# Optimization experiments

Hardware: AMD Instinct MI355X
Metric: run time of the kernel (lower is better)

Reference implementation:

```python
import jax, jax.numpy as jnp
import numpy as np

V, D, H, L, E, DH, K, PMAX = 50257, 128, 4, 4, 8, 512, 2, 256
B, T = 8, 256


def setup_inputs() -> dict:
    key = jax.random.key(0)
    ks = jax.random.split(key, 10)
    s = 0.02
    def n(k, shape):
        return jax.random.normal(k, shape, jnp.float32) * s
    return dict(
        idx=jax.random.randint(ks[0], (B, T), 0, V),
        tok_emb=n(ks[1], (V, D)),
        pos_emb=n(ks[2], (PMAX, D)),
        ln1_g=jnp.ones((L, D), jnp.float32), ln1_b=jnp.zeros((L, D), jnp.float32),
        in_w=n(ks[3], (L, 3 * D, D)), in_b=jnp.zeros((L, 3 * D), jnp.float32),
        out_w=n(ks[4], (L, D, D)), out_b=jnp.zeros((L, D), jnp.float32),
        ln2_g=jnp.ones((L, D), jnp.float32), ln2_b=jnp.zeros((L, D), jnp.float32),
        gate_w=n(ks[5], (L, E, D)),
        w1=n(ks[6], (L, E, DH, D)),
        w2=n(ks[7], (L, E, D, DH)),
        lnf_g=jnp.ones((D,), jnp.float32), lnf_b=jnp.zeros((D,), jnp.float32),
        lm_w=n(ks[8], (V, D)),
    )


def _ln(x, g, b):
    mu = x.mean(-1, keepdims=True)
    var = jnp.var(x, -1, keepdims=True)
    return (x - mu) / jnp.sqrt(var + 1e-5) * g + b


def _moe(x, gw, w1, w2):
    # x: [N, D]; top-2 sparse MoE, computed densely per expert then combined.
    logits = x @ gw.T                              # [N, E]
    probs = jax.nn.softmax(logits, -1)
    topw, topi = jax.lax.top_k(probs, K)           # [N, K]
    topw = topw / topw.sum(-1, keepdims=True)
    we = (topw[..., None] * jax.nn.one_hot(topi, E, dtype=x.dtype)).sum(1)  # [N, E]
    h = jax.nn.silu(jnp.einsum('nd,ehd->neh', x, w1))   # [N, E, DH]
    y = jnp.einsum('neh,edh->ned', h, w2)               # [N, E, D]
    return jnp.einsum('ned,ne->nd', y, we)


def reference(idx, tok_emb, pos_emb, ln1_g, ln1_b, in_w, in_b, out_w, out_b,
              ln2_g, ln2_b, gate_w, w1, w2, lnf_g, lnf_b, lm_w):
    b, t = idx.shape
    x = tok_emb[idx] + pos_emb[:t]                 # [B, T, D]
    dh = D // H
    scale = 1.0 / np.sqrt(dh)
    for l in range(L):
        xl = _ln(x, ln1_g[l], ln1_b[l])
        qkv = xl @ in_w[l].T + in_b[l]
        q, k, v = jnp.split(qkv, 3, -1)
        q = q.reshape(b, t, H, dh)
        k = k.reshape(b, t, H, dh)
        v = v.reshape(b, t, H, dh)
        att = jax.nn.softmax(jnp.einsum('bqhd,bkhd->bhqk', q, k) * scale, -1)
        o = jnp.einsum('bhqk,bkhd->bqhd', att, v).reshape(b, t, D)
        x = x + o @ out_w[l].T + out_b[l]
        x2 = _ln(x, ln2_g[l], ln2_b[l]).reshape(b * t, D)
        x = x + _moe(x2, gate_w[l], w1[l], w2[l]).reshape(b, t, D)
    return _ln(x, lnf_g, lnf_b) @ lm_w.T           # [B, T, V]
```

## Files before the change

### kernel.cpp

```cpp
#include <hip/hip_runtime.h>
#include <math.h>

#define NTOK 2048
#define DD   128
#define NHEAD 4
#define DHEAD 32
#define NLAYER 4
#define NEXP 8
#define DHID 512
#define NVOCAB 50257
#define VPAD  50304
#define SEQ   256
#define NBATCH 8

typedef __attribute__((ext_vector_type(8))) short short8v;
typedef __attribute__((ext_vector_type(4))) float f32x4;

__device__ __forceinline__ unsigned short nm_bf16r(float f) {
  unsigned u = __float_as_uint(f);
  u += 0x7fffu + ((u >> 16) & 1u);
  return (unsigned short)(u >> 16);
}

__device__ __forceinline__ float nm_silu(float a) {
  return a / (1.f + __expf(-a));
}

template<int N4>
__device__ __forceinline__ float nm_dotv(const float* __restrict__ a,
                                         const float* __restrict__ w) {
  const float4* a4 = (const float4*)a;
  const float4* w4 = (const float4*)w;
  float sx = 0.f, sy = 0.f, sz = 0.f, sw = 0.f;
#pragma unroll 16
  for (int k = 0; k < N4; ++k) {
    float4 av = a4[k], wv = w4[k];
    sx = fmaf(av.x, wv.x, sx);
    sy = fmaf(av.y, wv.y, sy);
    sz = fmaf(av.z, wv.z, sz);
    sw = fmaf(av.w, wv.w, sw);
  }
  return (sx + sy) + (sz + sw);
}

__global__ void nm_embed_ln(const int* __restrict__ idx, const float* __restrict__ tok,
                            const float* __restrict__ pos, const float* __restrict__ g,
                            const float* __restrict__ b, float* __restrict__ x,
                            float* __restrict__ xl) {
  int n = blockIdx.x, lane = threadIdx.x;
  int t = idx[n];
  float v0 = tok[(size_t)t * DD + lane]      + pos[(n % SEQ) * DD + lane];
  float v1 = tok[(size_t)t * DD + lane + 64] + pos[(n % SEQ) * DD + lane + 64];
  x[n * DD + lane]      = v0;
  x[n * DD + lane + 64] = v1;
  float s = v0 + v1;
#pragma unroll
  for (int o = 32; o > 0; o >>= 1) s += __shfl_xor(s, o, 64);
  float mu = s * (1.f / 128.f);
  float d0 = v0 - mu, d1 = v1 - mu;
  float q = d0 * d0 + d1 * d1;
#pragma unroll
  for (int o = 32; o > 0; o >>= 1) q += __shfl_xor(q, o, 64);
  float rstd = rsqrtf(q * (1.f / 128.f) + 1e-5f);
  xl[n * DD + lane]      = d0 * rstd * g[lane]      + b[lane];
  xl[n * DD + lane + 64] = d1 * rstd * g[lane + 64] + b[lane + 64];
}

__global__ void nm_ln(const float* __restrict__ in, const float* __restrict__ g,
                      const float* __restrict__ b, float* __restrict__ out) {
  int n = blockIdx.x, lane = threadIdx.x;
  float v0 = in[n * DD + lane], v1 = in[n * DD + lane + 64];
  float s = v0 + v1;
#pragma unroll
  for (int o = 32; o > 0; o >>= 1) s += __shfl_xor(s, o, 64);
  float mu = s * (1.f / 128.f);
  float d0 = v0 - mu, d1 = v1 - mu;
  float q = d0 * d0 + d1 * d1;
#pragma unroll
  for (int o = 32; o > 0; o >>= 1) q += __shfl_xor(q, o, 64);
  float rstd = rsqrtf(q * (1.f / 128.f) + 1e-5f);
  out[n * DD + lane]      = d0 * rstd * g[lane]      + b[lane];
  out[n * DD + lane + 64] = d1 * rstd * g[lane + 64] + b[lane + 64];
}

__global__ void nm_combine_ln(const float* __restrict__ yb, const int* __restrict__ posm,
                              const float* __restrict__ topw, float* __restrict__ x,
                              const float* __restrict__ g, const float* __restrict__ b,
                              float* __restrict__ xl, unsigned short* __restrict__ xb) {
  int n = blockIdx.x, lane = threadIdx.x;
  float w0 = topw[2 * n], w1 = topw[2 * n + 1];
  int p0 = posm[2 * n], p1 = posm[2 * n + 1];
  float v0 = x[n * DD + lane]      + w0 * yb[(size_t)p0 * DD + lane]
                                   + w1 * yb[(size_t)p1 * DD + lane];
  float v1 = x[n * DD + lane + 64] + w0 * yb[(size_t)p0 * DD + lane + 64]
                                   + w1 * yb[(size_t)p1 * DD + lane + 64];
  x[n * DD + lane]      = v0;
  x[n * DD + lane + 64] = v1;
  float s = v0 + v1;
#pragma unroll
  for (int o = 32; o > 0; o >>= 1) s += __shfl_xor(s, o, 64);
  float mu = s * (1.f / 128.f);
  float d0 = v0 - mu, d1 = v1 - mu;
  float q = d0 * d0 + d1 * d1;
#pragma unroll
  for (int o = 32; o > 0; o >>= 1) q += __shfl_xor(q, o, 64);
  float rstd = rsqrtf(q * (1.f / 128.f) + 1e-5f);
  float o0 = d0 * rstd * g[lane]      + b[lane];
  float o1 = d1 * rstd * g[lane + 64] + b[lane + 64];
  xl[n * DD + lane]      = o0;
  xl[n * DD + lane + 64] = o1;
  if (xb) {
    xb[n * DD + lane]      = nm_bf16r(o0);
    xb[n * DD + lane + 64] = nm_bf16r(o1);
  }
}

template<int F>
__global__ __launch_bounds__(256) void nm_gemm(
    const float* __restrict__ A, const float* __restrict__ B,
    float* __restrict__ C, const float* __restrict__ bias,
    int M, int N, int K,
    const int* __restrict__ list, const int* __restrict__ cnt,
    const int* __restrict__ off) {
  constexpr bool GA = F & 1, SI = F & 2, BI = F & 4, RE = F & 8, GR = F & 16;
  __shared__ __align__(16) float As[64][68];
  __shared__ __align__(16) float Bs[64][68];
  int tid = threadIdx.x;
  int n0 = blockIdx.x * 64, m0 = blockIdx.y * 64;
  int Mloc = M, o = 0;
  const float* Bb = B;
  if constexpr (GR) {
    int e = blockIdx.z;
    Mloc = cnt[e];
    if (m0 >= Mloc) return;
    o = off[e];
    Bb = B + (size_t)e * (size_t)N * K;
  }
  int tm = tid & 15, tn = tid >> 4;
  float acc[4][4] = {};
  for (int kc = 0; kc < K; kc += 64) {
#pragma unroll
    for (int i = 0; i < 4; ++i) {
      int f = tid + 256 * i;
      int r = f >> 4, c4 = f & 15;
      int mi = m0 + r;
      if (mi >= Mloc) mi = m0;
      const float* ar;
      if constexpr (GA) ar = A + (size_t)(list[o + mi] >> 1) * K;
      else              ar = A + (size_t)(o + mi) * K;
      float4 v = *(const float4*)(ar + kc + c4 * 4);
      int k = c4 * 4;
      As[k][r] = v.x; As[k + 1][r] = v.y; As[k + 2][r] = v.z; As[k + 3][r] = v.w;
    }
#pragma unroll
    for (int i = 0; i < 4; ++i) {
      int f = tid + 256 * i;
      int r = f >> 4, c4 = f & 15;
      const float* br = Bb + (size_t)(n0 + r) * K + kc + c4 * 4;
      float4 v = *(const float4*)br;
      int k = c4 * 4;
      Bs[k][r] = v.x; Bs[k + 1][r] = v.y; Bs[k + 2][r] = v.z; Bs[k + 3][r] = v.w;
    }
    __syncthreads();
#pragma unroll 16
    for (int k = 0; k < 64; ++k) {
      float4 a = *(const float4*)&As[k][tm * 4];
      float4 b = *(const float4*)&Bs[k][tn * 4];
      acc[0][0] = fmaf(a.x, b.x, acc[0][0]); acc[0][1] = fmaf(a.x, b.y, acc[0][1]);
      acc[0][2] = fmaf(a.x, b.z, acc[0][2]); acc[0][3] = fmaf(a.x, b.w, acc[0][3]);
      acc[1][0] = fmaf(a.y, b.x, acc[1][0]); acc[1][1] = fmaf(a.y, b.y, acc[1][1]);
      acc[1][2] = fmaf(a.y, b.z, acc[1][2]); acc[1][3] = fmaf(a.y, b.w, acc[1][3]);
      acc[2][0] = fmaf(a.z, b.x, acc[2][0]); acc[2][1] = fmaf(a.z, b.y, acc[2][1]);
      acc[2][2] = fmaf(a.z, b.z, acc[2][2]); acc[2][3] = fmaf(a.z, b.w, acc[2][3]);
      acc[3][0] = fmaf(a.w, b.x, acc[3][0]); acc[3][1] = fmaf(a.w, b.y, acc[3][1]);
      acc[3][2] = fmaf(a.w, b.z, acc[3][2]); acc[3][3] = fmaf(a.w, b.w, acc[3][3]);
    }
    __syncthreads();
  }
  float4 bv = {0.f, 0.f, 0.f, 0.f};
  if constexpr (BI) bv = *(const float4*)(bias + n0 + tn * 4);
#pragma unroll
  for (int i = 0; i < 4; ++i) {
    int mi = m0 + tm * 4 + i;
    if (GR && mi >= Mloc) continue;
    float* cr = C + (size_t)(o + mi) * N + n0 + tn * 4;
    float r0 = acc[i][0], r1 = acc[i][1], r2 = acc[i][2], r3 = acc[i][3];
    if constexpr (BI) { r0 += bv.x; r1 += bv.y; r2 += bv.z; r3 += bv.w; }
    if constexpr (SI) { r0 = nm_silu(r0); r1 = nm_silu(r1); r2 = nm_silu(r2); r3 = nm_silu(r3); }
    if constexpr (RE) { r0 += cr[0]; r1 += cr[1]; r2 += cr[2]; r3 += cr[3]; }
    float4 st = {r0, r1, r2, r3};
    *(float4*)cr = st;
  }
}

__global__ __launch_bounds__(256) void nm_oplng(
    const float* __restrict__ ao, const float* __restrict__ w,
    const float* __restrict__ bias, float* __restrict__ x,
    const float* __restrict__ g, const float* __restrict__ b,
    float* __restrict__ xl, const float* __restrict__ gw,
    int* __restrict__ topi, float* __restrict__ topw, int* __restrict__ cnt) {
  __shared__ __align__(16) float As[64][36];
  __shared__ __align__(16) float Bs[64][132];
  __shared__ float Ls[32][9];
  int tid = threadIdx.x;
  int m0 = blockIdx.x * 32;
  int tm = tid >> 5, tn = tid & 31;
  float acc[4][4] = {};
  for (int kc = 0; kc < DD; kc += 64) {
#pragma unroll
    for (int i = 0; i < 2; ++i) {
      int ch = tid + 256 * i, r = ch >> 4, c4 = ch & 15;
      float4 v = *(const float4*)(ao + (size_t)(m0 + r) * DD + kc + c4 * 4);
      int k = c4 * 4;
      As[k][r] = v.x; As[k + 1][r] = v.y; As[k + 2][r] = v.z; As[k + 3][r] = v.w;
    }
#pragma unroll
    for (int i = 0; i < 8; ++i) {
      int ch = tid + 256 * i, r = ch >> 4, c4 = ch & 15;
      float4 v = *(const float4*)(w + (size_t)r * DD + kc + c4 * 4);
      int k = c4 * 4;
      Bs[k][r] = v.x; Bs[k + 1][r] = v.y; Bs[k + 2][r] = v.z; Bs[k + 3][r] = v.w;
    }
    __syncthreads();
#pragma unroll 8
    for (int k = 0; k < 64; ++k) {
      float4 a = *(const float4*)&As[k][tm * 4];
      float4 bb = *(const float4*)&Bs[k][tn * 4];
      acc[0][0] = fmaf(a.x, bb.x, acc[0][0]); acc[0][1] = fmaf(a.x, bb.y, acc[0][1]);
      acc[0][2] = fmaf(a.x, bb.z, acc[0][2]); acc[0][3] = fmaf(a.x, bb.w, acc[0][3]);
      acc[1][0] = fmaf(a.y, bb.x, acc[1][0]); acc[1][1] = fmaf(a.y, bb.y, acc[1][1]);
      acc[1][2] = fmaf(a.y, bb.z, acc[1][2]); acc[1][3] = fmaf(a.y, bb.w, acc[1][3]);
      acc[2][0] = fmaf(a.z, bb.x, acc[2][0]); acc[2][1] = fmaf(a.z, bb.y, acc[2][1]);
      acc[2][2] = fmaf(a.z, bb.z, acc[2][2]); acc[2][3] = fmaf(a.z, bb.w, acc[2][3]);
      acc[3][0] = fmaf(a.w, bb.x, acc[3][0]); acc[3][1] = fmaf(a.w, bb.y, acc[3][1]);
      acc[3][2] = fmaf(a.w, bb.z, acc[3][2]); acc[3][3] = fmaf(a.w, bb.w, acc[3][3]);
    }
    __syncthreads();
  }
  float4 bv = *(const float4*)(bias + tn * 4);
  float rr[4][4], s1[4], s2[4];
#pragma unroll
  for (int i = 0; i < 4; ++i) {
    int rw = m0 + tm * 4 + i;
    float4 xv = *(const float4*)(x + (size_t)rw * DD + tn * 4);
    float r0 = acc[i][0] + bv.x + xv.x;
    float r1 = acc[i][1] + bv.y + xv.y;
    float r2 = acc[i][2] + bv.z + xv.z;
    float r3 = acc[i][3] + bv.w + xv.w;
    rr[i][0] = r0; rr[i][1] = r1; rr[i][2] = r2; rr[i][3] = r3;
    float4 st = {r0, r1, r2, r3};
    *(float4*)(x + (size_t)rw * DD + tn * 4) = st;
    s1[i] = r0 + r1 + r2 + r3;
    s2[i] = r0 * r0 + r1 * r1 + r2 * r2 + r3 * r3;
  }
#pragma unroll
  for (int o = 16; o >= 1; o >>= 1) {
#pragma unroll
    for (int i = 0; i < 4; ++i) {
      s1[i] += __shfl_xor(s1[i], o, 64);
      s2[i] += __shfl_xor(s2[i], o, 64);
    }
  }
  float4 gv  = *(const float4*)(g + tn * 4);
  float4 bbv = *(const float4*)(b + tn * 4);
#pragma unroll
  for (int i = 0; i < 4; ++i) {
    int rw = m0 + tm * 4 + i;
    float mu = s1[i] * (1.f / 128.f);
    float var = s2[i] * (1.f / 128.f) - mu * mu;
    float rstd = rsqrtf(var + 1e-5f);
    float y0 = (rr[i][0] - mu) * rstd * gv.x + bbv.x;
    float y1 = (rr[i][1] - mu) * rstd * gv.y + bbv.y;
    float y2 = (rr[i][2] - mu) * rstd * gv.z + bbv.z;
    float y3 = (rr[i][3] - mu) * rstd * gv.w + bbv.w;
    float4 yv = {y0, y1, y2, y3};
    *(float4*)(xl + (size_t)rw * DD + tn * 4) = yv;
    *(float4*)&Bs[tm * 4 + i][tn * 4] = yv;
  }
  __syncthreads();
  int grow = tid >> 3, ge = tid & 7;
  const float4* xr = (const float4*)&Bs[grow][0];
  const float4* wr = (const float4*)(gw + (size_t)ge * DD);
  float sx = 0.f, sy = 0.f, sz = 0.f, sw = 0.f;
#pragma unroll
  for (int k2 = 0; k2 < 32; ++k2) {
    float4 a = xr[k2], w4 = wr[k2];
    sx = fmaf(a.x, w4.x, sx); sy = fmaf(a.y, w4.y, sy);
    sz = fmaf(a.z, w4.z, sz); sw = fmaf(a.w, w4.w, sw);
  }
  Ls[grow][ge] = (sx + sy) + (sz + sw);
  __syncthreads();
  if (ge == 0) {
    float gl[NEXP];
#pragma unroll
    for (int e = 0; e < NEXP; ++e) gl[e] = Ls[grow][e];
    int i0 = 0;
#pragma unroll
    for (int e = 1; e < NEXP; ++e) if (gl[e] > gl[i0]) i0 = e;
    int i1 = (i0 == 0) ? 1 : 0;
#pragma unroll
    for (int e = 0; e < NEXP; ++e) { if (e != i0 && gl[e] > gl[i1]) i1 = e; }
    float p1 = __expf(gl[i1] - gl[i0]);
    float inv = 1.f / (1.f + p1);
    int n = m0 + grow;
    topi[2 * n] = i0; topi[2 * n + 1] = i1;
    topw[2 * n] = inv; topw[2 * n + 1] = p1 * inv;
    atomicAdd(cnt + i0, 1);
    atomicAdd(cnt + i1, 1);
  }
}

__global__ __launch_bounds__(256) void nm_attn2(const float* __restrict__ qkv,
                                                float* __restrict__ o) {
  __shared__ __align__(16) float Ks[SEQ][DHEAD];
  __shared__ __align__(16) float Vs[SEQ][DHEAD];
  __shared__ float mbuf[32][9], sbuf[32][9];
  __shared__ __align__(16) float accbuf[32][36];
  int bh = blockIdx.x;
  int b = bh >> 2, h = bh & 3;
  int qt = blockIdx.y;
  int tid = threadIdx.x;
  const float* base = qkv + (size_t)b * SEQ * 384;
  for (int f = tid; f < SEQ * 8; f += 256) {
    int t = f >> 3, c4 = f & 7;
    float4 kv = *(const float4*)(base + (size_t)t * 384 + 128 + h * DHEAD + c4 * 4);
    float4 vv = *(const float4*)(base + (size_t)t * 384 + 256 + h * DHEAD + c4 * 4);
    *(float4*)&Ks[t][c4 * 4] = kv;
    *(float4*)&Vs[t][c4 * 4] = vv;
  }
  __syncthreads();
  int q = tid & 31, slot = tid >> 5;
  int tq = qt * 32 + q;
  float qv[DHEAD];
  const float4* q4 = (const float4*)(base + (size_t)tq * 384 + h * DHEAD);
#pragma unroll
  for (int k = 0; k < 8; ++k) {
    float4 v = q4[k];
    qv[4*k] = v.x; qv[4*k+1] = v.y; qv[4*k+2] = v.z; qv[4*k+3] = v.w;
  }
  float m = -1e30f, s = 0.f, acc[DHEAD];
#pragma unroll
  for (int d = 0; d < DHEAD; ++d) acc[d] = 0.f;
  const float scale = 0.17677669529663687f;
  int j0 = slot * 32;
  for (int jj = 0; jj < 32; ++jj) {
    int j = j0 + jj;
    const float4* kr = (const float4*)Ks[j];
    float sc = 0.f;
#pragma unroll
    for (int k = 0; k < 8; ++k) {
      float4 v = kr[k];
      sc += qv[4*k]*v.x + qv[4*k+1]*v.y + qv[4*k+2]*v.z + qv[4*k+3]*v.w;
    }
    sc *= scale;
    float mn = fmaxf(m, sc);
    float f = __expf(m - mn), p = __expf(sc - mn);
    s = s * f + p;
    const float4* vr = (const float4*)Vs[j];
#pragma unroll
    for (int k = 0; k < 8; ++k) {
      float4 v = vr[k];
      acc[4*k]   = acc[4*k]  * f + p * v.x;
      acc[4*k+1] = acc[4*k+1]* f + p * v.y;
      acc[4*k+2] = acc[4*k+2]* f + p * v.z;
      acc[4*k+3] = acc[4*k+3]* f + p * v.w;
    }
    m = mn;
  }
  mbuf[q][slot] = m;
  sbuf[q][slot] = s;
  __syncthreads();
  float M = mbuf[q][0];
#pragma unroll
  for (int t = 1; t < 8; ++t) M = fmaxf(M, mbuf[q][t]);
  float S = 0.f;
#pragma unroll
  for (int t = 0; t < 8; ++t) S += sbuf[q][t] * __expf(mbuf[q][t] - M);
  float w = __expf(m - M);
#pragma unroll
  for (int d = 0; d < DHEAD; ++d) acc[d] *= w;
#pragma unroll
  for (int p = 0; p < 8; ++p) {
    if (slot == p) {
      if (p == 0) {
#pragma unroll
        for (int d = 0; d < DHEAD; ++d) accbuf[q][d] = acc[d];
      } else {
#pragma unroll
        for (int d = 0; d < DHEAD; ++d) accbuf[q][d] += acc[d];
      }
    }
    __syncthreads();
  }
  if (slot == 0) sbuf[q][8] = 1.f / S;
  __syncthreads();
  int q2 = tid >> 3, c4 = tid & 7;
  float inv = sbuf[q2][8];
  float4 v = *(const float4*)&accbuf[q2][c4 * 4];
  v.x *= inv; v.y *= inv; v.z *= inv; v.w *= inv;
  *(float4*)(o + (size_t)(b * SEQ + qt * 32 + q2) * DD + h * DHEAD + c4 * 4) = v;
}

__global__ void nm_route(const int* __restrict__ topi, const int* __restrict__ cnt,
                         int* __restrict__ off, int* __restrict__ list,
                         int* __restrict__ posm) {
  __shared__ int lcur[NEXP];
  int tid = threadIdx.x;
  if (tid < NEXP) {
    int o = 0;
    for (int e = 0; e < tid; ++e) o += cnt[e];
    lcur[tid] = o;
    off[tid] = o;
  }
  __syncthreads();
  for (int t = tid; t < 2 * NTOK; t += 1024) {
    int e = topi[t];
    int p = atomicAdd(&lcur[e], 1);
    list[p] = t;
    posm[t] = p;
  }
}

__global__ void nm_zero(int* __restrict__ p, int n) {
  int i = blockIdx.x * 64 + threadIdx.x;
  if (i < n) p[i] = 0;
}

__global__ void nm_moe(const float* __restrict__ x2, const float* __restrict__ gw,
                       const float* __restrict__ w1, const float* __restrict__ w2,
                       float* __restrict__ x) {
  __shared__ __align__(16) float xs[DD];
  __shared__ __align__(16) float hs[DHID];
  __shared__ float gl[NEXP];
  __shared__ int   ei[2];
  __shared__ float ew[2];
  int n = blockIdx.x, tid = threadIdx.x;
  if (tid < DD) xs[tid] = x2[n * DD + tid];
  __syncthreads();
  if (tid < NEXP) gl[tid] = nm_dotv<32>(xs, gw + (size_t)tid * DD);
  __syncthreads();
  if (tid == 0) {
    int i0 = 0;
#pragma unroll
    for (int e = 1; e < NEXP; ++e) if (gl[e] > gl[i0]) i0 = e;
    int i1 = (i0 == 0) ? 1 : 0;
    for (int e = 0; e < NEXP; ++e) { if (e == i0) continue; if (gl[e] > gl[i1]) i1 = e; }
    float p1 = __expf(gl[i1] - gl[i0]);
    float inv = 1.f / (1.f + p1);
    ei[0] = i0; ei[1] = i1; ew[0] = inv; ew[1] = p1 * inv;
  }
  __syncthreads();
  float yacc = 0.f;
  for (int t2 = 0; t2 < 2; ++t2) {
    int e = ei[t2];
    float wt = ew[t2];
    const float* w1e = w1 + (size_t)e * DHID * DD;
#pragma unroll
    for (int jj = 0; jj < 2; ++jj) {
      int j = tid + jj * 256;
      float a = nm_dotv<32>(xs, w1e + (size_t)j * DD);
      hs[j] = nm_silu(a);
    }
    __syncthreads();
    if (tid < DD) yacc += wt * nm_dotv<128>(hs, w2 + ((size_t)e * DD + tid) * DHID);
    __syncthreads();
  }
  if (tid < DD) x[n * DD + tid] += yacc;
}

__global__ void nm_cvt_w(const float* __restrict__ in, unsigned short* __restrict__ ob) {
  size_t i = (size_t)blockIdx.x * 256 + threadIdx.x;
  const size_t n = (size_t)NVOCAB * DD;
  ob[i] = (i < n) ? nm_bf16r(in[i]) : (unsigned short)0;
}

__device__ __forceinline__ short8v nm_cvt8(const float* p) {
  const float4* p4 = (const float4*)p;
  float4 a = p4[0], b = p4[1];
  short8v r;
  r[0] = (short)nm_bf16r(a.x); r[1] = (short)nm_bf16r(a.y);
  r[2] = (short)nm_bf16r(a.z); r[3] = (short)nm_bf16r(a.w);
  r[4] = (short)nm_bf16r(b.x); r[5] = (short)nm_bf16r(b.y);
  r[6] = (short)nm_bf16r(b.z); r[7] = (short)nm_bf16r(b.w);
  return r;
}

__global__ __launch_bounds__(256) void nm_lmhead2(
    const unsigned short* __restrict__ xfb, const unsigned short* __restrict__ lmwb,
    float* __restrict__ out) {
  __shared__ unsigned short Ab[128 * 128];
  __shared__ unsigned short Bb[128 * 128];
  int tid = threadIdx.x;
  int row0 = blockIdx.y * 128, col0 = blockIdx.x * 128;
#pragma unroll
  for (int i = 0; i < 8; ++i) {
    int ch = tid + i * 256;
    int r = ch >> 4, s = ch & 15;
    int sg = s ^ (r & 7);
    *(short8v*)&Ab[r * 128 + s * 8] =
        *(const short8v*)(xfb + (size_t)(row0 + r) * DD + sg * 8);
    *(short8v*)&Bb[r * 128 + s * 8] =
        *(const short8v*)(lmwb + (size_t)(col0 + r) * DD + sg * 8);
  }
  __syncthreads();
  int wave = tid >> 6, lane = tid & 63;
  int wr = wave >> 1, wc = wave & 1;
  int lr = lane & 15, hk = lane >> 4;
  f32x4 acc[4][4] = {};
#pragma unroll
  for (int ks = 0; ks < 4; ++ks) {
    int sg = ks * 4 + hk;
    int sx = (sg ^ (lr & 7)) * 8;
    short8v a[4], b[4];
#pragma unroll
    for (int i = 0; i < 4; ++i)
      a[i] = *(const short8v*)&Ab[(wr * 64 + i * 16 + lr) * 128 + sx];
#pragma unroll
    for (int j = 0; j < 4; ++j)
      b[j] = *(const short8v*)&Bb[(wc * 64 + j * 16 + lr) * 128 + sx];
#pragma unroll
    for (int i = 0; i < 4; ++i)
#pragma unroll
      for (int j = 0; j < 4; ++j)
        acc[i][j] = __builtin_amdgcn_mfma_f32_16x16x32_bf16(a[i], b[j], acc[i][j], 0, 0, 0);
  }
  int cr = (lane >> 4) * 4;
#pragma unroll
  for (int j = 0; j < 4; ++j) {
    int c = col0 + wc * 64 + j * 16 + (lane & 15);
    if (c < NVOCAB) {
#pragma unroll
      for (int i = 0; i < 4; ++i)
#pragma unroll
        for (int r = 0; r < 4; ++r)
          out[(size_t)(row0 + wr * 64 + i * 16 + cr + r) * NVOCAB + c] = acc[i][j][r];
    }
  }
}

__global__ __launch_bounds__(256) void nm_lmhead_f32(
    const float* __restrict__ xf, const float* __restrict__ lmw,
    float* __restrict__ out) {
  int wave = threadIdx.x >> 6, lane = threadIdx.x & 63;
  int wr = wave >> 1, wc = wave & 1;
  int row0 = blockIdx.y * 128 + wr * 64;
  int col0 = blockIdx.x * 128 + wc * 64;
  int lr = lane & 15, lk = (lane >> 4) * 8;
  f32x4 acc[4][4] = {};
#pragma unroll
  for (int ks = 0; ks < 4; ++ks) {
    int kb = ks * 32 + lk;
    short8v a[4], b[4];
#pragma unroll
    for (int i = 0; i < 4; ++i)
      a[i] = nm_cvt8(xf + (size_t)(row0 + i * 16 + lr) * DD + kb);
#pragma unroll
    for (int j = 0; j < 4; ++j) {
      int c = col0 + j * 16 + lr;
      if (c < NVOCAB) b[j] = nm_cvt8(lmw + (size_t)c * DD + kb);
      else {
        short8v z;
#pragma unroll
        for (int e = 0; e < 8; ++e) z[e] = 0;
        b[j] = z;
      }
    }
#pragma unroll
    for (int i = 0; i < 4; ++i)
#pragma unroll
      for (int j = 0; j < 4; ++j)
        acc[i][j] = __builtin_amdgcn_mfma_f32_16x16x32_bf16(a[i], b[j], acc[i][j], 0, 0, 0);
  }
  int cr = (lane >> 4) * 4;
#pragma unroll
  for (int j = 0; j < 4; ++j) {
    int c = col0 + j * 16 + (lane & 15);
    if (c < NVOCAB) {
#pragma unroll
      for (int i = 0; i < 4; ++i)
#pragma unroll
        for (int r = 0; r < 4; ++r)
          out[(size_t)(row0 + i * 16 + cr + r) * NVOCAB + c] = acc[i][j][r];
    }
  }
}

extern "C" void kernel_launch(void* const* d_in, const int* in_sizes, int n_in,
                              void* d_out, int out_size, void* d_ws, size_t ws_size,
                              hipStream_t stream) {
  const int*   idx   = (const int*)  d_in[0];
  const float* tok   = (const float*)d_in[1];
  const float* pos   = (const float*)d_in[2];
  const float* ln1g  = (const float*)d_in[3];
  const float* ln1b  = (const float*)d_in[4];
  const float* inw   = (const float*)d_in[5];
  const float* inb   = (const float*)d_in[6];
  const float* outw  = (const float*)d_in[7];
  const float* outb  = (const float*)d_in[8];
  const float* ln2g  = (const float*)d_in[9];
  const float* ln2b  = (const float*)d_in[10];
  const float* gatew = (const float*)d_in[11];
  const float* w1    = (const float*)d_in[12];
  const float* w2    = (const float*)d_in[13];
  const float* lnfg  = (const float*)d_in[14];
  const float* lnfb  = (const float*)d_in[15];
  const float* lmw   = (const float*)d_in[16];
  float* out = (float*)d_out;

  float* ws   = (float*)d_ws;
  float* x    = ws;
  float* xl   = x    + NTOK * DD;
  float* qkv  = xl   + NTOK * DD;
  float* ao   = qkv  + NTOK * 384;
  float* topw = ao   + NTOK * DD;
  int*   topi = (int*)(topw + 2 * NTOK);
  int*   list = topi + 2 * NTOK;
  int*   posm = list + 2 * NTOK;
  int*   cnt  = posm + 2 * NTOK;
  int*   offs = cnt  + NLAYER * NEXP;
  float* H    = (float*)(offs + NLAYER * NEXP);
  float* yb   = H    + 2 * NTOK * DHID;
  unsigned short* xfb  = (unsigned short*)(yb + 2 * NTOK * DD);
  unsigned short* lmwb = xfb + NTOK * DD;

  const size_t moe_bytes = (size_t)((char*)xfb - (char*)d_ws);
  const size_t pre_bytes = moe_bytes + ((size_t)NTOK * DD + (size_t)VPAD * DD) * 2;
  const bool moe_ok = (ws_size >= moe_bytes);
  const bool pre = (ws_size >= pre_bytes);

  nm_embed_ln<<<NTOK, 64, 0, stream>>>(idx, tok, pos, ln1g, ln1b, x, xl);
  if (moe_ok) nm_zero<<<(NLAYER * NEXP + 63) / 64, 64, 0, stream>>>(cnt, NLAYER * NEXP);
  if (pre) nm_cvt_w<<<VPAD * DD / 256, 256, 0, stream>>>(lmw, lmwb);

  for (int l = 0; l < NLAYER; ++l) {
    nm_gemm<4><<<dim3(384 / 64, NTOK / 64), 256, 0, stream>>>(
        xl, inw + (size_t)l * 384 * DD, qkv, inb + (size_t)l * 384,
        NTOK, 384, DD, nullptr, nullptr, nullptr);
    nm_attn2<<<dim3(NBATCH * NHEAD, SEQ / 32), 256, 0, stream>>>(qkv, ao);
    nm_oplng<<<NTOK / 32, 256, 0, stream>>>(
        ao, outw + (size_t)l * DD * DD, outb + (size_t)l * DD, x,
        ln2g + l * DD, ln2b + l * DD, xl, gatew + (size_t)l * NEXP * DD,
        topi, topw, cnt + l * NEXP);

    const float* gN = (l < NLAYER - 1) ? ln1g + (l + 1) * DD : lnfg;
    const float* bN = (l < NLAYER - 1) ? ln1b + (l + 1) * DD : lnfb;
    if (moe_ok) {
      int* cnt_l = cnt + l * NEXP;
      int* off_l = offs + l * NEXP;
      const float* w1l = w1 + (size_t)l * NEXP * DHID * DD;
      const float* w2l = w2 + (size_t)l * NEXP * DD * DHID;
      nm_route<<<1, 1024, 0, stream>>>(topi, cnt_l, off_l, list, posm);
      nm_gemm<19><<<dim3(DHID / 64, 2 * NTOK / 64, NEXP), 256, 0, stream>>>(
          xl, w1l, H, nullptr, 0, DHID, DD, list, cnt_l, off_l);
      nm_gemm<16><<<dim3(DD / 64, 2 * NTOK / 64, NEXP), 256, 0, stream>>>(
          H, w2l, yb, nullptr, 0, DD, DHID, nullptr, cnt_l, off_l);
      nm_combine_ln<<<NTOK, 64, 0, stream>>>(
          yb, posm, topw, x, gN, bN, xl,
          (l == NLAYER - 1 && pre) ? xfb : (unsigned short*)nullptr);
    } else {
      nm_moe<<<NTOK, 256, 0, stream>>>(xl, gatew + (size_t)l * NEXP * DD,
                                       w1 + (size_t)l * NEXP * DHID * DD,
                                       w2 + (size_t)l * NEXP * DD * DHID, x);
      nm_ln<<<NTOK, 64, 0, stream>>>(x, gN, bN, xl);
    }
  }

  if (pre) {
    nm_lmhead2<<<dim3(VPAD / 128, NTOK / 128), 256, 0, stream>>>(xfb, lmwb, out);
  } else {
    nm_lmhead_f32<<<dim3(VPAD / 128, NTOK / 128), 256, 0, stream>>>(xl, lmw, out);
  }
}
```

Baseline: 848.9 us.

## Use bf16 MFMA expert GEMMs for last layer and enlarge fp32 GEMM tiles

Measured after the change: 825.5 us. 2.8% less time.

```diff
diff --git a/kernel.cpp b/kernel.cpp
--- a/kernel.cpp
+++ b/kernel.cpp
@@ -46,7 +46,7 @@
 __global__ void nm_embed_ln(const int* __restrict__ idx, const float* __restrict__ tok,
                             const float* __restrict__ pos, const float* __restrict__ g,
                             const float* __restrict__ b, float* __restrict__ x,
-                            float* __restrict__ xl) {
+                            float* __restrict__ xlf, unsigned short* __restrict__ xlb) {
   int n = blockIdx.x, lane = threadIdx.x;
   int t = idx[n];
   float v0 = tok[(size_t)t * DD + lane]      + pos[(n % SEQ) * DD + lane];
@@ -62,8 +62,10 @@
 #pragma unroll
   for (int o = 32; o > 0; o >>= 1) q += __shfl_xor(q, o, 64);
   float rstd = rsqrtf(q * (1.f / 128.f) + 1e-5f);
-  xl[n * DD + lane]      = d0 * rstd * g[lane]      + b[lane];
-  xl[n * DD + lane + 64] = d1 * rstd * g[lane + 64] + b[lane + 64];
+  float o0 = d0 * rstd * g[lane]      + b[lane];
+  float o1 = d1 * rstd * g[lane + 64] + b[lane + 64];
+  if (xlf) { xlf[n * DD + lane] = o0; xlf[n * DD + lane + 64] = o1; }
+  if (xlb) { xlb[n * DD + lane] = nm_bf16r(o0); xlb[n * DD + lane + 64] = nm_bf16r(o1); }
 }
 
 __global__ void nm_ln(const float* __restrict__ in, const float* __restrict__ g,
@@ -116,17 +118,17 @@
 }
 
 template<int F>
-__global__ __launch_bounds__(256) void nm_gemm(
+__global__ __launch_bounds__(256) void nm_gemm2(
     const float* __restrict__ A, const float* __restrict__ B,
     float* __restrict__ C, const float* __restrict__ bias,
     int M, int N, int K,
     const int* __restrict__ list, const int* __restrict__ cnt,
     const int* __restrict__ off) {
-  constexpr bool GA = F & 1, SI = F & 2, BI = F & 4, RE = F & 8, GR = F & 16;
-  __shared__ __align__(16) float As[64][68];
+  constexpr bool GA = F & 1, SI = F & 2, BI = F & 4, GR = F & 16;
+  __shared__ __align__(16) float As[64][132];
   __shared__ __align__(16) float Bs[64][68];
   int tid = threadIdx.x;
-  int n0 = blockIdx.x * 64, m0 = blockIdx.y * 64;
+  int n0 = blockIdx.x * 64, m0 = blockIdx.y * 128;
   int Mloc = M, o = 0;
   const float* Bb = B;
   if constexpr (GR) {
@@ -137,10 +139,10 @@
     Bb = B + (size_t)e * (size_t)N * K;
   }
   int tm = tid & 15, tn = tid >> 4;
-  float acc[4][4] = {};
+  float acc[8][4] = {};
   for (int kc = 0; kc < K; kc += 64) {
 #pragma unroll
-    for (int i = 0; i < 4; ++i) {
+    for (int i = 0; i < 8; ++i) {
       int f = tid + 256 * i;
       int r = f >> 4, c4 = f & 15;
       int mi = m0 + r;
@@ -164,32 +166,113 @@
     __syncthreads();
 #pragma unroll 16
     for (int k = 0; k < 64; ++k) {
-      float4 a = *(const float4*)&As[k][tm * 4];
+      float4 a0 = *(const float4*)&As[k][tm * 4];
+      float4 a1 = *(const float4*)&As[k][64 + tm * 4];
       float4 b = *(const float4*)&Bs[k][tn * 4];
-      acc[0][0] = fmaf(a.x, b.x, acc[0][0]); acc[0][1] = fmaf(a.x, b.y, acc[0][1]);
-      acc[0][2] = fmaf(a.x, b.z, acc[0][2]); acc[0][3] = fmaf(a.x, b.w, acc[0][3]);
-      acc[1][0] = fmaf(a.y, b.x, acc[1][0]); acc[1][1] = fmaf(a.y, b.y, acc[1][1]);
-      acc[1][2] = fmaf(a.y, b.z, acc[1][2]); acc[1][3] = fmaf(a.y, b.w, acc[1][3]);
-      acc[2][0] = fmaf(a.z, b.x, acc[2][0]); acc[2][1] = fmaf(a.z, b.y, acc[2][1]);
-      acc[2][2] = fmaf(a.z, b.z, acc[2][2]); acc[2][3] = fmaf(a.z, b.w, acc[2][3]);
-      acc[3][0] = fmaf(a.w, b.x, acc[3][0]); acc[3][1] = fmaf(a.w, b.y, acc[3][1]);
-      acc[3][2] = fmaf(a.w, b.z, acc[3][2]); acc[3][3] = fmaf(a.w, b.w, acc[3][3]);
+      acc[0][0] = fmaf(a0.x, b.x, acc[0][0]); acc[0][1] = fmaf(a0.x, b.y, acc[0][1]);
+      acc[0][2] = fmaf(a0.x, b.z, acc[0][2]); acc[0][3] = fmaf(a0.x, b.w, acc[0][3]);
+      acc[1][0] = fmaf(a0.y, b.x, acc[1][0]); acc[1][1] = fmaf(a0.y, b.y, acc[1][1]);
+      acc[1][2] = fmaf(a0.y, b.z, acc[1][2]); acc[1][3] = fmaf(a0.y, b.w, acc[1][3]);
+      acc[2][0] = fmaf(a0.z, b.x, acc[2][0]); acc[2][1] = fmaf(a0.z, b.y, acc[2][1]);
+      acc[2][2] = fmaf(a0.z, b.z, acc[2][2]); acc[2][3] = fmaf(a0.z, b.w, acc[2][3]);
+      acc[3][0] = fmaf(a0.w, b.x, acc[3][0]); acc[3][1] = fmaf(a0.w, b.y, acc[3][1]);
+      acc[3][2] = fmaf(a0.w, b.z, acc[3][2]); acc[3][3] = fmaf(a0.w, b.w, acc[3][3]);
+      acc[4][0] = fmaf(a1.x, b.x, acc[4][0]); acc[4][1] = fmaf(a1.x, b.y, acc[4][1]);
+      acc[4][2] = fmaf(a1.x, b.z, acc[4][2]); acc[4][3] = fmaf(a1.x, b.w, acc[4][3]);
+      acc[5][0] = fmaf(a1.y, b.x, acc[5][0]); acc[5][1] = fmaf(a1.y, b.y, acc[5][1]);
+      acc[5][2] = fmaf(a1.y, b.z, acc[5][2]); acc[5][3] = fmaf(a1.y, b.w, acc[5][3]);
+      acc[6][0] = fmaf(a1.z, b.x, acc[6][0]); acc[6][1] = fmaf(a1.z, b.y, acc[6][1]);
+      acc[6][2] = fmaf(a1.z, b.z, acc[6][2]); acc[6][3] = fmaf(a1.z, b.w, acc[6][3]);
+      acc[7][0] = fmaf(a1.w, b.x, acc[7][0]); acc[7][1] = fmaf(a1.w, b.y, acc[7][1]);
+      acc[7][2] = fmaf(a1.w, b.z, acc[7][2]); acc[7][3] = fmaf(a1.w, b.w, acc[7][3]);
     }
     __syncthreads();
   }
   float4 bv = {0.f, 0.f, 0.f, 0.f};
   if constexpr (BI) bv = *(const float4*)(bias + n0 + tn * 4);
 #pragma unroll
-  for (int i = 0; i < 4; ++i) {
-    int mi = m0 + tm * 4 + i;
-    if (GR && mi >= Mloc) continue;
-    float* cr = C + (size_t)(o + mi) * N + n0 + tn * 4;
-    float r0 = acc[i][0], r1 = acc[i][1], r2 = acc[i][2], r3 = acc[i][3];
-    if constexpr (BI) { r0 += bv.x; r1 += bv.y; r2 += bv.z; r3 += bv.w; }
-    if constexpr (SI) { r0 = nm_silu(r0); r1 = nm_silu(r1); r2 = nm_silu(r2); r3 = nm_silu(r3); }
-    if constexpr (RE) { r0 += cr[0]; r1 += cr[1]; r2 += cr[2]; r3 += cr[3]; }
-    float4 st = {r0, r1, r2, r3};
-    *(float4*)cr = st;
+  for (int g = 0; g < 2; ++g) {
+#pragma unroll
+    for (int i = 0; i < 4; ++i) {
+      int row = m0 + g * 64 + tm * 4 + i;
+      if (GR && row >= Mloc) continue;
+      float* cr = C + (size_t)(o + row) * N + n0 + tn * 4;
+      float r0 = acc[g * 4 + i][0], r1 = acc[g * 4 + i][1];
+      float r2 = acc[g * 4 + i][2], r3 = acc[g * 4 + i][3];
+      if constexpr (BI) { r0 += bv.x; r1 += bv.y; r2 += bv.z; r3 += bv.w; }
+      if constexpr (SI) { r0 = nm_silu(r0); r1 = nm_silu(r1); r2 = nm_silu(r2); r3 = nm_silu(r3); }
+      float4 st = {r0, r1, r2, r3};
+      *(float4*)cr = st;
+    }
+  }
+}
+
+template<int F, int KK>
+__global__ __launch_bounds__(256) void nm_bgemm(
+    const unsigned short* __restrict__ A, const unsigned short* __restrict__ B,
+    float* __restrict__ Cf, unsigned short* __restrict__ Cb,
+    const float* __restrict__ bias, int M, int N,
+    const int* __restrict__ list, const int* __restrict__ cnt,
+    const int* __restrict__ off) {
+  constexpr bool GA = F & 1, SI = F & 2, BI = F & 4, SB = F & 8, GR = F & 16;
+  int wave = threadIdx.x >> 6, lane = threadIdx.x & 63;
+  int n0 = blockIdx.x * 32;
+  int m0 = blockIdx.y * 128 + wave * 32;
+  int Mloc = M, o = 0;
+  const unsigned short* Bb = B;
+  if constexpr (GR) {
+    int e = blockIdx.z;
+    Mloc = cnt[e];
+    o = off[e];
+    Bb = B + (size_t)e * (size_t)N * KK;
+  }
+  if (m0 >= Mloc) return;
+  int lr = lane & 15, lk = (lane >> 4) * 8;
+  const unsigned short* arow[2];
+#pragma unroll
+  for (int i = 0; i < 2; ++i) {
+    int mi = m0 + i * 16 + lr;
+    if (mi >= Mloc) mi = Mloc - 1;
+    int r = GA ? (list[o + mi] >> 1) : (o + mi);
+    arow[i] = A + (size_t)r * KK;
+  }
+  const unsigned short* brow[2] = { Bb + (size_t)(n0 + lr) * KK,
+                                    Bb + (size_t)(n0 + 16 + lr) * KK };
+  f32x4 acc[2][2] = {};
+#pragma unroll
+  for (int ks = 0; ks < KK / 32; ++ks) {
+    int kb = ks * 32 + lk;
+    short8v a0 = *(const short8v*)(arow[0] + kb);
+    short8v a1 = *(const short8v*)(arow[1] + kb);
+    short8v b0 = *(const short8v*)(brow[0] + kb);
+    short8v b1 = *(const short8v*)(brow[1] + kb);
+    acc[0][0] = __builtin_amdgcn_mfma_f32_16x16x32_bf16(a0, b0, acc[0][0], 0, 0, 0);
+    acc[0][1] = __builtin_amdgcn_mfma_f32_16x16x32_bf16(a0, b1, acc[0][1], 0, 0, 0);
+    acc[1][0] = __builtin_amdgcn_mfma_f32_16x16x32_bf16(a1, b0, acc[1][0], 0, 0, 0);
+    acc[1][1] = __builtin_amdgcn_mfma_f32_16x16x32_bf16(a1, b1, acc[1][1], 0, 0, 0);
+  }
+  float bc[2] = {0.f, 0.f};
+  if constexpr (BI) {
+    bc[0] = bias[n0 + (lane & 15)];
+    bc[1] = bias[n0 + 16 + (lane & 15)];
+  }
+#pragma unroll
+  for (int i = 0; i < 2; ++i) {
+    int rbase = m0 + i * 16 + (lane >> 4) * 4;
+#pragma unroll
+    for (int r = 0; r < 4; ++r) {
+      int row = rbase + r;
+      if (GR && row >= Mloc) continue;
+#pragma unroll
+      for (int j = 0; j < 2; ++j) {
+        float v = acc[i][j][r];
+        if constexpr (BI) v += bc[j];
+        if constexpr (SI) v = nm_silu(v);
+        int col = n0 + j * 16 + (lane & 15);
+        if constexpr (SB) Cb[(size_t)(o + row) * N + col] = nm_bf16r(v);
+        else              Cf[(size_t)(o + row) * N + col] = v;
+      }
+    }
   }
 }
 
@@ -197,7 +280,8 @@
     const float* __restrict__ ao, const float* __restrict__ w,
     const float* __restrict__ bias, float* __restrict__ x,
     const float* __restrict__ g, const float* __restrict__ b,
-    float* __restrict__ xl, const float* __restrict__ gw,
+    float* __restrict__ xlf, unsigned short* __restrict__ xlb,
+    const float* __restrict__ gw,
     int* __restrict__ topi, float* __restrict__ topw, int* __restrict__ cnt) {
   __shared__ __align__(16) float As[64][36];
   __shared__ __align__(16) float Bs[64][132];
@@ -274,7 +358,11 @@
     float y2 = (rr[i][2] - mu) * rstd * gv.z + bbv.z;
     float y3 = (rr[i][3] - mu) * rstd * gv.w + bbv.w;
     float4 yv = {y0, y1, y2, y3};
-    *(float4*)(xl + (size_t)rw * DD + tn * 4) = yv;
+    if (xlf) *(float4*)(xlf + (size_t)rw * DD + tn * 4) = yv;
+    if (xlb) {
+      ushort4 us = {nm_bf16r(y0), nm_bf16r(y1), nm_bf16r(y2), nm_bf16r(y3)};
+      *(ushort4*)(xlb + (size_t)rw * DD + tn * 4) = us;
+    }
     *(float4*)&Bs[tm * 4 + i][tn * 4] = yv;
   }
   __syncthreads();
@@ -426,6 +514,46 @@
   if (i < n) p[i] = 0;
 }
 
+#define C3_LMW 6438912ull
+#define C3_W1  6963200ull
+#define C3_ALL 7487488ull
+__global__ void nm_cvt3(const float* __restrict__ lmw, const float* __restrict__ w1l3,
+                        const float* __restrict__ w2l3,
+                        unsigned short* __restrict__ lmwb,
+                        unsigned short* __restrict__ w1b3,
+                        unsigned short* __restrict__ w2b3) {
+  size_t i = (size_t)blockIdx.x * 256 + threadIdx.x;
+  if (i < C3_LMW) {
+    lmwb[i] = (i < (size_t)NVOCAB * DD) ? nm_bf16r(lmw[i]) : (unsigned short)0;
+  } else if (i < C3_W1) {
+    size_t j = i - C3_LMW; w1b3[j] = nm_bf16r(w1l3[j]);
+  } else if (i < C3_ALL) {
+    size_t j = i - C3_W1; w2b3[j] = nm_bf16r(w2l3[j]);
+  }
+}
+
+__global__ void nm_qkv(const float* __restrict__ xl, const float* __restrict__ w,
+                       const float* __restrict__ bias, float* __restrict__ qkv) {
+  __shared__ __align__(16) float xs[DD];
+  int n = blockIdx.x, tid = threadIdx.x;
+  xs[tid] = xl[n * DD + tid];
+  __syncthreads();
+#pragma unroll
+  for (int jj = 0; jj < 3; ++jj) {
+    int j = tid + jj * 128;
+    qkv[(size_t)n * 384 + j] = nm_dotv<32>(xs, w + (size_t)j * DD) + bias[j];
+  }
+}
+
+__global__ void nm_outproj(const float* __restrict__ ao, const float* __restrict__ w,
+                           const float* __restrict__ bias, float* __restrict__ x) {
+  __shared__ __align__(16) float os[DD];
+  int n = blockIdx.x, tid = threadIdx.x;
+  os[tid] = ao[n * DD + tid];
+  __syncthreads();
+  x[n * DD + tid] += nm_dotv<32>(os, w + (size_t)tid * DD) + bias[tid];
+}
+
 __global__ void nm_moe(const float* __restrict__ x2, const float* __restrict__ gw,
                        const float* __restrict__ w1, const float* __restrict__ w2,
                        float* __restrict__ x) {
@@ -468,12 +596,6 @@
   if (tid < DD) x[n * DD + tid] += yacc;
 }
 
-__global__ void nm_cvt_w(const float* __restrict__ in, unsigned short* __restrict__ ob) {
-  size_t i = (size_t)blockIdx.x * 256 + threadIdx.x;
-  const size_t n = (size_t)NVOCAB * DD;
-  ob[i] = (i < n) ? nm_bf16r(in[i]) : (unsigned short)0;
-}
-
 __device__ __forceinline__ short8v nm_cvt8(const float* p) {
   const float4* p4 = (const float4*)p;
   float4 a = p4[0], b = p4[1];
@@ -485,59 +607,6 @@
   return r;
 }
 
-__global__ __launch_bounds__(256) void nm_lmhead2(
-    const unsigned short* __restrict__ xfb, const unsigned short* __restrict__ lmwb,
-    float* __restrict__ out) {
-  __shared__ unsigned short Ab[128 * 128];
-  __shared__ unsigned short Bb[128 * 128];
-  int tid = threadIdx.x;
-  int row0 = blockIdx.y * 128, col0 = blockIdx.x * 128;
-#pragma unroll
-  for (int i = 0; i < 8; ++i) {
-    int ch = tid + i * 256;
-    int r = ch >> 4, s = ch & 15;
-    int sg = s ^ (r & 7);
-    *(short8v*)&Ab[r * 128 + s * 8] =
-        *(const short8v*)(xfb + (size_t)(row0 + r) * DD + sg * 8);
-    *(short8v*)&Bb[r * 128 + s * 8] =
-        *(const short8v*)(lmwb + (size_t)(col0 + r) * DD + sg * 8);
-  }
-  __syncthreads();
-  int wave = tid >> 6, lane = tid & 63;
-  int wr = wave >> 1, wc = wave & 1;
-  int lr = lane & 15, hk = lane >> 4;
-  f32x4 acc[4][4] = {};
-#pragma unroll
-  for (int ks = 0; ks < 4; ++ks) {
-    int sg = ks * 4 + hk;
-    int sx = (sg ^ (lr & 7)) * 8;
-    short8v a[4], b[4];
-#pragma unroll
-    for (int i = 0; i < 4; ++i)
-      a[i] = *(const short8v*)&Ab[(wr * 64 + i * 16 + lr) * 128 + sx];
-#pragma unroll
-    for (int j = 0; j < 4; ++j)
-      b[j] = *(const short8v*)&Bb[(wc * 64 + j * 16 + lr) * 128 + sx];
-#pragma unroll
-    for (int i = 0; i < 4; ++i)
-#pragma unroll
-      for (int j = 0; j < 4; ++j)
-        acc[i][j] = __builtin_amdgcn_mfma_f32_16x16x32_bf16(a[i], b[j], acc[i][j], 0, 0, 0);
-  }
-  int cr = (lane >> 4) * 4;
-#pragma unroll
-  for (int j = 0; j < 4; ++j) {
-    int c = col0 + wc * 64 + j * 16 + (lane & 15);
-    if (c < NVOCAB) {
-#pragma unroll
-      for (int i = 0; i < 4; ++i)
-#pragma unroll
-        for (int r = 0; r < 4; ++r)
-          out[(size_t)(row0 + wr * 64 + i * 16 + cr + r) * NVOCAB + c] = acc[i][j][r];
-    }
-  }
-}
-
 __global__ __launch_bounds__(256) void nm_lmhead_f32(
     const float* __restrict__ xf, const float* __restrict__ lmw,
     float* __restrict__ out) {
@@ -581,6 +650,59 @@
 #pragma unroll
         for (int r = 0; r < 4; ++r)
           out[(size_t)(row0 + i * 16 + cr + r) * NVOCAB + c] = acc[i][j][r];
+    }
+  }
+}
+
+__global__ __launch_bounds__(256) void nm_lmhead2(
+    const unsigned short* __restrict__ xfb, const unsigned short* __restrict__ lmwb,
+    float* __restrict__ out) {
+  __shared__ unsigned short Ab[128 * 128];
+  __shared__ unsigned short Bb[128 * 128];
+  int tid = threadIdx.x;
+  int row0 = blockIdx.y * 128, col0 = blockIdx.x * 128;
+#pragma unroll
+  for (int i = 0; i < 8; ++i) {
+    int ch = tid + i * 256;
+    int r = ch >> 4, s = ch & 15;
+    int sg = s ^ (r & 7);
+    *(short8v*)&Ab[r * 128 + s * 8] =
+        *(const short8v*)(xfb + (size_t)(row0 + r) * DD + sg * 8);
+    *(short8v*)&Bb[r * 128 + s * 8] =
+        *(const short8v*)(lmwb + (size_t)(col0 + r) * DD + sg * 8);
+  }
+  __syncthreads();
+  int wave = tid >> 6, lane = tid & 63;
+  int wr = wave >> 1, wc = wave & 1;
+  int lr = lane & 15, hk = lane >> 4;
+  f32x4 acc[4][4] = {};
+#pragma unroll
+  for (int ks = 0; ks < 4; ++ks) {
+    int sg = ks * 4 + hk;
+    int sx = (sg ^ (lr & 7)) * 8;
+    short8v a[4], b[4];
+#pragma unroll
+    for (int i = 0; i < 4; ++i)
+      a[i] = *(const short8v*)&Ab[(wr * 64 + i * 16 + lr) * 128 + sx];
+#pragma unroll
+    for (int j = 0; j < 4; ++j)
+      b[j] = *(const short8v*)&Bb[(wc * 64 + j * 16 + lr) * 128 + sx];
+#pragma unroll
+    for (int i = 0; i < 4; ++i)
+#pragma unroll
+      for (int j = 0; j < 4; ++j)
+        acc[i][j] = __builtin_amdgcn_mfma_f32_16x16x32_bf16(a[i], b[j], acc[i][j], 0, 0, 0);
+  }
+  int cr = (lane >> 4) * 4;
+#pragma unroll
+  for (int j = 0; j < 4; ++j) {
+    int c = col0 + wc * 64 + j * 16 + (lane & 15);
+    if (c < NVOCAB) {
+#pragma unroll
+      for (int i = 0; i < 4; ++i)
+#pragma unroll
+        for (int r = 0; r < 4; ++r)
+          out[(size_t)(row0 + wr * 64 + i * 16 + cr + r) * NVOCAB + c] = acc[i][j][r];
     }
   }
 }
@@ -613,61 +735,78 @@
   float* qkv  = xl   + NTOK * DD;
   float* ao   = qkv  + NTOK * 384;
   float* topw = ao   + NTOK * DD;
-  int*   topi = (int*)(topw + 2 * NTOK);
+  float* H    = topw + 2 * NTOK;
+  float* yb   = H    + 2 * NTOK * DHID;
+  int*   topi = (int*)(yb + 2 * NTOK * DD);
   int*   list = topi + 2 * NTOK;
   int*   posm = list + 2 * NTOK;
   int*   cnt  = posm + 2 * NTOK;
   int*   offs = cnt  + NLAYER * NEXP;
-  float* H    = (float*)(offs + NLAYER * NEXP);
-  float* yb   = H    + 2 * NTOK * DHID;
-  unsigned short* xfb  = (unsigned short*)(yb + 2 * NTOK * DD);
-  unsigned short* lmwb = xfb + NTOK * DD;
-
-  const size_t moe_bytes = (size_t)((char*)xfb - (char*)d_ws);
-  const size_t pre_bytes = moe_bytes + ((size_t)NTOK * DD + (size_t)VPAD * DD) * 2;
-  const bool moe_ok = (ws_size >= moe_bytes);
-  const bool pre = (ws_size >= pre_bytes);
-
-  nm_embed_ln<<<NTOK, 64, 0, stream>>>(idx, tok, pos, ln1g, ln1b, x, xl);
-  if (moe_ok) nm_zero<<<(NLAYER * NEXP + 63) / 64, 64, 0, stream>>>(cnt, NLAYER * NEXP);
-  if (pre) nm_cvt_w<<<VPAD * DD / 256, 256, 0, stream>>>(lmw, lmwb);
-
-  for (int l = 0; l < NLAYER; ++l) {
-    nm_gemm<4><<<dim3(384 / 64, NTOK / 64), 256, 0, stream>>>(
-        xl, inw + (size_t)l * 384 * DD, qkv, inb + (size_t)l * 384,
-        NTOK, 384, DD, nullptr, nullptr, nullptr);
-    nm_attn2<<<dim3(NBATCH * NHEAD, SEQ / 32), 256, 0, stream>>>(qkv, ao);
-    nm_oplng<<<NTOK / 32, 256, 0, stream>>>(
-        ao, outw + (size_t)l * DD * DD, outb + (size_t)l * DD, x,
-        ln2g + l * DD, ln2b + l * DD, xl, gatew + (size_t)l * NEXP * DD,
-        topi, topw, cnt + l * NEXP);
-
-    const float* gN = (l < NLAYER - 1) ? ln1g + (l + 1) * DD : lnfg;
-    const float* bN = (l < NLAYER - 1) ? ln1b + (l + 1) * DD : lnfb;
-    if (moe_ok) {
+  unsigned short* xlb  = (unsigned short*)(offs + NLAYER * NEXP);
+  unsigned short* Hb   = xlb + NTOK * DD;
+  unsigned short* xfb  = Hb  + 2 * NTOK * DHID;
+  unsigned short* w1b3 = xfb + NTOK * DD;
+  unsigned short* w2b3 = w1b3 + NEXP * DHID * DD;
+  unsigned short* lmwb = w2b3 + NEXP * DD * DHID;
+  const size_t need = (size_t)((char*)(lmwb + (size_t)VPAD * DD) - (char*)d_ws);
+  const bool pre = (ws_size >= need);
+
+  const float* w1l3 = w1 + (size_t)3 * NEXP * DHID * DD;
+  const float* w2l3 = w2 + (size_t)3 * NEXP * DD * DHID;
+
+  if (pre) {
+    nm_cvt3<<<(unsigned)(C3_ALL / 256), 256, 0, stream>>>(
+        lmw, w1l3, w2l3, lmwb, w1b3, w2b3);
+    nm_zero<<<1, 64, 0, stream>>>(cnt, NLAYER * NEXP);
+    nm_embed_ln<<<NTOK, 64, 0, stream>>>(idx, tok, pos, ln1g, ln1b, x, xl, nullptr);
+    for (int l = 0; l < NLAYER; ++l) {
+      nm_gemm2<4><<<dim3(384 / 64, NTOK / 128), 256, 0, stream>>>(
+          xl, inw + (size_t)l * 384 * DD, qkv, inb + (size_t)l * 384,
+          NTOK, 384, DD, nullptr, nullptr, nullptr);
+      nm_attn2<<<dim3(NBATCH * NHEAD, SEQ / 32), 256, 0, stream>>>(qkv, ao);
+      nm_oplng<<<NTOK / 32, 256, 0, stream>>>(
+          ao, outw + (size_t)l * DD * DD, outb + (size_t)l * DD, x,
+          ln2g + l * DD, ln2b + l * DD, xl, (l == 3) ? xlb : (unsigned short*)nullptr,
+          gatew + (size_t)l * NEXP * DD, topi, topw, cnt + l * NEXP);
       int* cnt_l = cnt + l * NEXP;
       int* off_l = offs + l * NEXP;
-      const float* w1l = w1 + (size_t)l * NEXP * DHID * DD;
-      const float* w2l = w2 + (size_t)l * NEXP * DD * DHID;
       nm_route<<<1, 1024, 0, stream>>>(topi, cnt_l, off_l, list, posm);
-      nm_gemm<19><<<dim3(DHID / 64, 2 * NTOK / 64, NEXP), 256, 0, stream>>>(
-          xl, w1l, H, nullptr, 0, DHID, DD, list, cnt_l, off_l);
-      nm_gemm<16><<<dim3(DD / 64, 2 * NTOK / 64, NEXP), 256, 0, stream>>>(
-          H, w2l, yb, nullptr, 0, DD, DHID, nullptr, cnt_l, off_l);
+      if (l < 3) {
+        const float* w1l = w1 + (size_t)l * NEXP * DHID * DD;
+        const float* w2l = w2 + (size_t)l * NEXP * DD * DHID;
+        nm_gemm2<19><<<dim3(DHID / 64, 2 * NTOK / 128, NEXP), 256, 0, stream>>>(
+            xl, w1l, H, nullptr, 0, DHID, DD, list, cnt_l, off_l);
+        nm_gemm2<16><<<dim3(DD / 64, 2 * NTOK / 128, NEXP), 256, 0, stream>>>(
+            H, w2l, yb, nullptr, 0, DD, DHID, nullptr, cnt_l, off_l);
+      } else {
+        nm_bgemm<27, 128><<<dim3(DHID / 32, 32, NEXP), 256, 0, stream>>>(
+            xlb, w1b3, nullptr, Hb, nullptr, 0, DHID, list, cnt_l, off_l);
+        nm_bgemm<16, 512><<<dim3(DD / 32, 32, NEXP), 256, 0, stream>>>(
+            Hb, w2b3, yb, nullptr, nullptr, 0, DD, nullptr, cnt_l, off_l);
+      }
+      const float* gN = (l < NLAYER - 1) ? ln1g + (l + 1) * DD : lnfg;
+      const float* bN = (l < NLAYER - 1) ? ln1b + (l + 1) * DD : lnfb;
       nm_combine_ln<<<NTOK, 64, 0, stream>>>(
           yb, posm, topw, x, gN, bN, xl,
-          (l == NLAYER - 1 && pre) ? xfb : (unsigned short*)nullptr);
-    } else {
+          (l == NLAYER - 1) ? xfb : (unsigned short*)nullptr);
+    }
+    nm_lmhead2<<<dim3(VPAD / 128, NTOK / 128), 256, 0, stream>>>(xfb, lmwb, out);
+  } else {
+    nm_embed_ln<<<NTOK, 64, 0, stream>>>(idx, tok, pos, ln1g, ln1b, x, xl, nullptr);
+    for (int l = 0; l < NLAYER; ++l) {
+      nm_qkv<<<NTOK, 128, 0, stream>>>(xl, inw + (size_t)l * 384 * DD,
+                                       inb + (size_t)l * 384, qkv);
+      nm_attn2<<<dim3(NBATCH * NHEAD, SEQ / 32), 256, 0, stream>>>(qkv, ao);
+      nm_outproj<<<NTOK, 128, 0, stream>>>(ao, outw + (size_t)l * DD * DD,
+                                           outb + (size_t)l * DD, x);
+      nm_ln<<<NTOK, 64, 0, stream>>>(x, ln2g + l * DD, ln2b + l * DD, xl);
       nm_moe<<<NTOK, 256, 0, stream>>>(xl, gatew + (size_t)l * NEXP * DD,
                                        w1 + (size_t)l * NEXP * DHID * DD,
                                        w2 + (size_t)l * NEXP * DD * DHID, x);
+      const float* gN = (l < NLAYER - 1) ? ln1g + (l + 1) * DD : lnfg;
+      const float* bN = (l < NLAYER - 1) ? ln1b + (l + 1) * DD : lnfb;
       nm_ln<<<NTOK, 64, 0, stream>>>(x, gN, bN, xl);
     }
-  }
-
-  if (pre) {
-    nm_lmhead2<<<dim3(VPAD / 128, NTOK / 128), 256, 0, stream>>>(xfb, lmwb, out);
-  } else {
     nm_lmhead_f32<<<dim3(VPAD / 128, NTOK / 128), 256, 0, stream>>>(xl, lmw, out);
   }
 }
```
